# Performance work log

Measured on AMD Instinct MI355X. Metric: run time of the kernel, lower is better.

Reference implementation:

```python
import jax, jax.numpy as jnp
import numpy as np

IN_F, OUT_F, GROUP = 4096, 4096, 128
N_GROUPS = IN_F // GROUP
NIB_SHIFTS = jnp.arange(8, dtype=jnp.int32) * 4  # 8 nibbles per int32


def dequantize(qweight, qzeros, scales, g_idx):
    """GPTQ/exllama 4-bit grouped dequant -> fp16 weight [K, N]."""
    # unpack qweight: [K//8, N] int32 -> [K//8, 8, N] nibbles -> [K, N]
    w_q = (qweight[:, None, :] >> NIB_SHIFTS[None, :, None]) & 0xF
    w_q = w_q.reshape(-1, qweight.shape[1])  # [K, N]
    # unpack qzeros: [G, N//8] int32 -> [G, N//8, 8] -> [G, N]
    z_q = (qzeros[:, :, None] >> NIB_SHIFTS[None, None, :]) & 0xF
    z_q = z_q.reshape(qzeros.shape[0], -1)  # [G, N]
    # exllama stores zero-points minus one: w = (q - (z + 1)) * scale
    z_rows = z_q[g_idx]            # [K, N] int32
    s_rows = scales[g_idx]         # [K, N] fp16
    return (w_q - z_rows - 1).astype(jnp.float16) * s_rows


def setup_inputs() -> dict:
    key = jax.random.key(0)
    k_x, k_qw, k_qz, k_s, k_b = jax.random.split(key, 5)
    x = jax.random.normal(k_x, (4, 2048, IN_F), dtype=jnp.float16)
    qweight = jax.random.randint(k_qw, (IN_F // 8, OUT_F), 0, 2147483647, dtype=jnp.int32)
    qzeros = jax.random.randint(k_qz, (N_GROUPS, OUT_F // 8), 0, 2147483647, dtype=jnp.int32)
    scales = (jax.random.uniform(k_s, (N_GROUPS, OUT_F), dtype=jnp.float32) * 0.01 + 0.001).astype(jnp.float16)
    g_idx = (jnp.arange(IN_F, dtype=jnp.int32) // GROUP).astype(jnp.int32)
    bias = (jax.random.normal(k_b, (OUT_F,), dtype=jnp.float32) * 0.02).astype(jnp.float16)
    return {"x": x, "qweight": qweight, "qzeros": qzeros, "scales": scales, "g_idx": g_idx, "bias": bias}


def reference(x, qweight, qzeros, scales, g_idx, bias):
    W = dequantize(qweight, qzeros, scales, g_idx)      # [K, N] fp16
    lead = x.shape[:-1]
    out = jnp.dot(x.reshape(-1, x.shape[-1]), W)        # fp16 GEMM, [T, N]
    out = out + bias
    return out.reshape(lead + (W.shape[1],))
```

## Files before the change

### kernel.cpp

```cpp
#include <hip/hip_runtime.h>
#include <hip/hip_bf16.h>
#include <stdint.h>

#define M_TOT 8192
#define N_TOT 4096
#define K_TOT 4096
#define GROUP 128


using f32x4  = __attribute__((ext_vector_type(4))) float;
using bf16x8 = __attribute__((ext_vector_type(8))) __bf16;

typedef __attribute__((address_space(3))) void as3_void;
typedef const __attribute__((address_space(1))) void as1_void;

__global__ __launch_bounds__(256) void prep(
    const float* __restrict__ x,
    const int*   __restrict__ qweight,
    const int*   __restrict__ qzeros,
    const float* __restrict__ scales,
    const int*   __restrict__ g_idx,
    __bf16* __restrict__ xb,
    __bf16* __restrict__ Wt)
{
    const int tid = threadIdx.x;
    if (blockIdx.x < 4096) {
        __shared__ __align__(16) unsigned short T[64 * 72];
        const int k0 = (blockIdx.x & 63) * 64;
        const int n0 = (blockIdx.x >> 6) * 64;
        const int g  = g_idx[k0];

        #pragma unroll
        for (int i = 0; i < 2; ++i) {
            const int idx = tid + i * 256;
            const int r   = idx >> 6;
            const int n   = idx & 63;
            const int qi  = qweight[(size_t)((k0 >> 3) + r) * N_TOT + n0 + n];
            const int zi  = qzeros[g * (N_TOT / 8) + ((n0 + n) >> 3)];
            const float s = scales[g * N_TOT + n0 + n];
            const float zs = (float)(((zi >> ((n & 7) * 4)) & 0xF) + 1) * s;
            bf16x8 v;
            #pragma unroll
            for (int j = 0; j < 8; ++j)
                v[j] = (__bf16)((float)((qi >> (4 * j)) & 0xF) * s - zs);
            *(bf16x8*)&T[n * 72 + r * 8] = v;
        }
        __syncthreads();

        const int n = tid >> 2;
        const int c = (tid & 3) * 16;
        const bf16x8 a = *(const bf16x8*)&T[n * 72 + c];
        const bf16x8 b = *(const bf16x8*)&T[n * 72 + c + 8];
        __bf16* dst = Wt + (size_t)(n0 + n) * K_TOT + k0 + c;
        *(bf16x8*)dst = a;
        *(bf16x8*)(dst + 8) = b;
    } else {
        const size_t t = (size_t)(blockIdx.x - 4096) * 256 + tid;
        const f32x4 f0 = __builtin_nontemporal_load((const f32x4*)(x + t * 8));
        const f32x4 f1 = __builtin_nontemporal_load((const f32x4*)(x + t * 8) + 1);
        bf16x8 v;
        v[0]=(__bf16)f0.x; v[1]=(__bf16)f0.y; v[2]=(__bf16)f0.z; v[3]=(__bf16)f0.w;
        v[4]=(__bf16)f1.x; v[5]=(__bf16)f1.y; v[6]=(__bf16)f1.z; v[7]=(__bf16)f1.w;
        *(bf16x8*)(xb + t * 8) = v;
    }
}

#define GBM 256
#define GBN 256
#define GBK 64
#define NKT (K_TOT / GBK)

#define BAR() do { asm volatile("" ::: "memory"); \
                   __builtin_amdgcn_s_barrier();  \
                   asm volatile("" ::: "memory"); } while (0)
#define WAIT_VM4()   asm volatile("s_waitcnt vmcnt(4)"   ::: "memory")
#define WAIT_VM0()   asm volatile("s_waitcnt vmcnt(0)"   ::: "memory")

#define GPHASE(q, STAGE_STMT, TAIL_STMT)                                      \
    {                                                                         \
        bf16x8 av[2][2];                                                      \
        _Pragma("unroll")                                                     \
        for (int ks = 0; ks < 2; ++ks) {                                      \
            av[0][ks] = ldfrag(&Abuf[buf][0], wm, 2 * (q), ks);               \
            av[1][ks] = ldfrag(&Abuf[buf][0], wm, 2 * (q) + 1, ks);           \
        }                                                                     \
        STAGE_STMT;                                                           \
        BAR();                                                                \
        __builtin_amdgcn_s_setprio(1);                                        \
        _Pragma("unroll")                                                     \
        for (int ks = 0; ks < 2; ++ks)                                        \
            _Pragma("unroll")                                                 \
            for (int mtl = 0; mtl < 2; ++mtl)                                 \
                _Pragma("unroll")                                             \
                for (int nt = 0; nt < 4; ++nt)                                \
                    acc[2 * (q) + mtl][nt] =                                  \
                        __builtin_amdgcn_mfma_f32_16x16x32_bf16(              \
                            av[mtl][ks], bv[nt][ks], acc[2 * (q) + mtl][nt],  \
                            0, 0, 0);                                         \
        __builtin_amdgcn_s_setprio(0);                                        \
        TAIL_STMT;                                                            \
        BAR();                                                                \
    }

__global__ __launch_bounds__(512, 2) void gemm8p(
    const __bf16* __restrict__ xb,
    const __bf16* __restrict__ Wt,
    const float*  __restrict__ bias,
    float* __restrict__ out)
{
    __shared__ __align__(16) unsigned short Abuf[2][GBM * GBK];
    __shared__ __align__(16) unsigned short Bbuf[2][GBM * GBK];

    const int tid  = threadIdx.x;
    const int wid  = tid >> 6;
    const int lane = tid & 63;
    const int l15  = lane & 15;
    const int quad = lane >> 4;

    int bid = blockIdx.x;
    bid = (bid & 7) * (512 >> 3) + (bid >> 3);
    const int tn = bid & (N_TOT / GBN - 1);
    const int tm = bid >> 4;
    const int m0 = tm * GBM;
    const int n0 = tn * GBN;

    const int wm = (wid >> 2) * 128;
    const int wn = (wid & 3) * 64;

    f32x4 acc[8][4];
    #pragma unroll
    for (int i = 0; i < 8; ++i)
        #pragma unroll
        for (int j = 0; j < 4; ++j)
            acc[i][j] = (f32x4)0.f;

    auto stage = [&](unsigned short* ldsb, int h,
                     const __bf16* __restrict__ base, int row0, int kt) {
        #pragma unroll
        for (int j = 0; j < 2; ++j) {
            const int c  = j * 512 + tid;
            const int rl = c >> 3;
            const int kc = (c & 7) ^ (rl & 7);
            const __bf16* ga = base + (size_t)(row0 + h * 128 + rl) * K_TOT
                             + kt * GBK + kc * 8;
            __builtin_amdgcn_global_load_lds((as1_void*)ga,
                (as3_void*)&ldsb[h * 8192 + (j * 512 + wid * 64) * 8],
                16, 0, 0);
        }
    };
    auto ldfrag = [&](const unsigned short* ldsb, int wbase, int mt,
                      int ks) -> bf16x8 {
        const int r = wbase + mt * 16 + l15;
        return *(const bf16x8*)
            &ldsb[r * GBK + (((ks * 4 + quad) ^ (r & 7)) << 3)];
    };

    stage(&Abuf[0][0], 0, xb, m0, 0); stage(&Abuf[0][0], 1, xb, m0, 0);
    stage(&Bbuf[0][0], 0, Wt, n0, 0); stage(&Bbuf[0][0], 1, Wt, n0, 0);
    stage(&Bbuf[1][0], 0, Wt, n0, 1); stage(&Bbuf[1][0], 1, Wt, n0, 1);
    WAIT_VM4();
    BAR();

    bf16x8 bv[4][2];

    for (int t = 0; t < NKT; ++t) {
        const int buf = t & 1;

        {
            #pragma unroll
            for (int nt = 0; nt < 4; ++nt)
                #pragma unroll
                for (int ks = 0; ks < 2; ++ks)
                    bv[nt][ks] = ldfrag(&Bbuf[buf][0], wn, nt, ks);
            bf16x8 av[2][2];
            #pragma unroll
            for (int ks = 0; ks < 2; ++ks) {
                av[0][ks] = ldfrag(&Abuf[buf][0], wm, 0, ks);
                av[1][ks] = ldfrag(&Abuf[buf][0], wm, 1, ks);
            }
            if (t + 1 < NKT) stage(&Abuf[buf ^ 1][0], 0, xb, m0, t + 1);
            BAR();
            __builtin_amdgcn_s_setprio(1);
            #pragma unroll
            for (int ks = 0; ks < 2; ++ks)
                #pragma unroll
                for (int mtl = 0; mtl < 2; ++mtl)
                    #pragma unroll
                    for (int nt = 0; nt < 4; ++nt)
                        acc[mtl][nt] = __builtin_amdgcn_mfma_f32_16x16x32_bf16(
                            av[mtl][ks], bv[nt][ks], acc[mtl][nt], 0, 0, 0);
            __builtin_amdgcn_s_setprio(0);
            BAR();
        }
        GPHASE(1, if (t + 1 < NKT) stage(&Abuf[buf ^ 1][0], 1, xb, m0, t + 1), );
        GPHASE(2, if (t + 2 < NKT) stage(&Bbuf[buf][0], 0, Wt, n0, t + 2), );
        GPHASE(3, if (t + 2 < NKT) stage(&Bbuf[buf][0], 1, Wt, n0, t + 2),
               if (t < NKT - 2) { WAIT_VM4(); } else { WAIT_VM0(); });
    }

    #pragma unroll
    for (int nt = 0; nt < 4; ++nt) {
        const int col = n0 + wn + nt * 16 + l15;
        const float bb = bias[col];
        #pragma unroll
        for (int mt = 0; mt < 8; ++mt) {
            const int rowb = m0 + wm + mt * 16 + quad * 4;
            #pragma unroll
            for (int i = 0; i < 4; ++i)
                out[(size_t)(rowb + i) * N_TOT + col] = acc[mt][nt][i] + bb;
        }
    }
}

#define FBM 256
#define FBN 128
#define FBKP 72

__global__ __launch_bounds__(256, 2) void gptq_gemm_fused(
    const float* __restrict__ x, const int* __restrict__ qweight,
    const int* __restrict__ qzeros, const float* __restrict__ scales,
    const int* __restrict__ g_idx, const float* __restrict__ bias,
    float* __restrict__ out)
{
    __shared__ __align__(16) unsigned short As[FBM * FBKP];
    __shared__ __align__(16) unsigned short Bt[FBN * FBKP];

    const int tid  = threadIdx.x;
    const int wave = tid >> 6;
    const int lane = tid & 63;
    const int n0 = blockIdx.x * FBN;
    const int m0 = blockIdx.y * FBM;
    const int wm = (wave >> 1) * 64;
    const int wn = (wave & 1) * 64;
    const int l15  = lane & 15;
    const int quad = lane >> 4;

    f32x4 acc[2][4][4];
    #pragma unroll
    for (int mi = 0; mi < 2; ++mi)
        #pragma unroll
        for (int i = 0; i < 4; ++i)
            #pragma unroll
            for (int j = 0; j < 4; ++j)
                acc[mi][i][j] = (f32x4)0.f;

    const int nb  = tid & 31;
    const int r   = tid >> 5;
    const int zsh = (nb & 7) * 4;

    for (int kt = 0; kt < K_TOT / 64; ++kt) {
        const int k0 = kt * 64;
        #pragma unroll
        for (int i = 0; i < 8; ++i) {
            const int c   = tid + i * 256;
            const int row = c >> 3;
            const int cb  = (c & 7) << 3;
            const float* xp = x + (size_t)(m0 + row) * K_TOT + (k0 + cb);
            const float4 f0 = *(const float4*)xp;
            const float4 f1 = *(const float4*)(xp + 4);
            bf16x8 v;
            v[0]=(__bf16)f0.x; v[1]=(__bf16)f0.y; v[2]=(__bf16)f0.z; v[3]=(__bf16)f0.w;
            v[4]=(__bf16)f1.x; v[5]=(__bf16)f1.y; v[6]=(__bf16)f1.z; v[7]=(__bf16)f1.w;
            *(bf16x8*)&As[row * FBKP + cb] = v;
        }
        const int g    = g_idx[k0];
        const int qrow = (k0 >> 3) + r;
        #pragma unroll
        for (int dn = 0; dn < 4; ++dn) {
            const int n  = nb + dn * 32;
            const int qi = qweight[(size_t)qrow * N_TOT + (n0 + n)];
            const int zi = qzeros[g * (N_TOT / 8) + ((n0 + n) >> 3)];
            const float s = scales[g * N_TOT + (n0 + n)];
            const float zs = (float)(((zi >> zsh) & 0xF) + 1) * s;
            bf16x8 v;
            #pragma unroll
            for (int j = 0; j < 8; ++j)
                v[j] = (__bf16)((float)((qi >> (4 * j)) & 0xF) * s - zs);
            *(bf16x8*)&Bt[n * FBKP + r * 8] = v;
        }
        __syncthreads();
        #pragma unroll
        for (int ks = 0; ks < 2; ++ks) {
            bf16x8 bvv[4];
            #pragma unroll
            for (int nt = 0; nt < 4; ++nt)
                bvv[nt] = *(const bf16x8*)&Bt[(wn + nt * 16 + l15) * FBKP + ks * 32 + quad * 8];
            #pragma unroll
            for (int mi = 0; mi < 2; ++mi) {
                bf16x8 av[4];
                #pragma unroll
                for (int mt = 0; mt < 4; ++mt)
                    av[mt] = *(const bf16x8*)&As[(mi * 128 + wm + mt * 16 + l15) * FBKP + ks * 32 + quad * 8];
                #pragma unroll
                for (int mt = 0; mt < 4; ++mt)
                    #pragma unroll
                    for (int nt = 0; nt < 4; ++nt)
                        acc[mi][mt][nt] = __builtin_amdgcn_mfma_f32_16x16x32_bf16(
                            av[mt], bvv[nt], acc[mi][mt][nt], 0, 0, 0);
            }
        }
        __syncthreads();
    }
    #pragma unroll
    for (int mi = 0; mi < 2; ++mi)
        #pragma unroll
        for (int nt = 0; nt < 4; ++nt) {
            const int col = n0 + wn + nt * 16 + l15;
            const float bvv = bias[col];
            #pragma unroll
            for (int mt = 0; mt < 4; ++mt) {
                const int rowb = m0 + mi * 128 + wm + mt * 16 + quad * 4;
                #pragma unroll
                for (int i = 0; i < 4; ++i)
                    out[(size_t)(rowb + i) * N_TOT + col] = acc[mi][mt][nt][i] + bvv;
            }
        }
}

extern "C" void kernel_launch(void* const* d_in, const int* in_sizes, int n_in,
                              void* d_out, int out_size, void* d_ws, size_t ws_size,
                              hipStream_t stream) {
    const float* x  = (const float*)d_in[0];
    const int*   qw = (const int*)d_in[1];
    const int*   qz = (const int*)d_in[2];
    const float* sc = (const float*)d_in[3];
    const int*   gi = (const int*)d_in[4];
    const float* bs = (const float*)d_in[5];
    float* out = (float*)d_out;

    const size_t xb_bytes = (size_t)M_TOT * K_TOT * 2;
    const size_t wt_bytes = (size_t)N_TOT * K_TOT * 2;

    if (ws_size >= xb_bytes + wt_bytes) {
        __bf16* xb = (__bf16*)d_ws;
        __bf16* Wt = (__bf16*)((char*)d_ws + xb_bytes);
        const int cast_blocks = (M_TOT * K_TOT) / (256 * 8);
        prep<<<dim3(4096 + cast_blocks), dim3(256), 0, stream>>>(
            x, qw, qz, sc, gi, xb, Wt);
        gemm8p<<<dim3((M_TOT / GBM) * (N_TOT / GBN)), dim3(512), 0, stream>>>(
            xb, Wt, bs, out);
    } else {
        gptq_gemm_fused<<<dim3(N_TOT / FBN, M_TOT / FBM), dim3(256), 0, stream>>>(
            x, qw, qz, sc, gi, bs, out);
    }
}
```

Measured before the change: 472.5 us.

## Restructure GEMM main loop with full double-buffering and register-prefetched A fragments

Both A and B tiles are now fully double-buffered, with stage t+2 loaded into the current buffer after it is consumed. Previously A used a one-step lookahead split across phases. A-fragment reads are ping-ponged between two register sets, so each phase's LDS reads overlap the previous phase's MFMAs, and an explicit lgkmcnt wait is added. This deepens the prefetch distance to hide global-load latency, at the cost of more registers and a vmcnt threshold that now depends on the exact count of in-flight loads.

```diff
diff --git a/kernel.cpp b/kernel.cpp
--- a/kernel.cpp
+++ b/kernel.cpp
@@ -73,34 +73,9 @@
 #define BAR() do { asm volatile("" ::: "memory"); \
                    __builtin_amdgcn_s_barrier();  \
                    asm volatile("" ::: "memory"); } while (0)
-#define WAIT_VM4()   asm volatile("s_waitcnt vmcnt(4)"   ::: "memory")
+#define WAIT_LGKM0() asm volatile("s_waitcnt lgkmcnt(0)" ::: "memory")
+#define WAIT_VM8()   asm volatile("s_waitcnt vmcnt(8)"   ::: "memory")
 #define WAIT_VM0()   asm volatile("s_waitcnt vmcnt(0)"   ::: "memory")
-
-#define GPHASE(q, STAGE_STMT, TAIL_STMT)                                      \
-    {                                                                         \
-        bf16x8 av[2][2];                                                      \
-        _Pragma("unroll")                                                     \
-        for (int ks = 0; ks < 2; ++ks) {                                      \
-            av[0][ks] = ldfrag(&Abuf[buf][0], wm, 2 * (q), ks);               \
-            av[1][ks] = ldfrag(&Abuf[buf][0], wm, 2 * (q) + 1, ks);           \
-        }                                                                     \
-        STAGE_STMT;                                                           \
-        BAR();                                                                \
-        __builtin_amdgcn_s_setprio(1);                                        \
-        _Pragma("unroll")                                                     \
-        for (int ks = 0; ks < 2; ++ks)                                        \
-            _Pragma("unroll")                                                 \
-            for (int mtl = 0; mtl < 2; ++mtl)                                 \
-                _Pragma("unroll")                                             \
-                for (int nt = 0; nt < 4; ++nt)                                \
-                    acc[2 * (q) + mtl][nt] =                                  \
-                        __builtin_amdgcn_mfma_f32_16x16x32_bf16(              \
-                            av[mtl][ks], bv[nt][ks], acc[2 * (q) + mtl][nt],  \
-                            0, 0, 0);                                         \
-        __builtin_amdgcn_s_setprio(0);                                        \
-        TAIL_STMT;                                                            \
-        BAR();                                                                \
-    }
 
 __global__ __launch_bounds__(512, 2) void gemm8p(
     const __bf16* __restrict__ xb,
@@ -108,8 +83,7 @@
     const float*  __restrict__ bias,
     float* __restrict__ out)
 {
-    __shared__ __align__(16) unsigned short Abuf[2][GBM * GBK];
-    __shared__ __align__(16) unsigned short Bbuf[2][GBM * GBK];
+    __shared__ __align__(16) unsigned short LDS[2][2][GBM * GBK];
 
     const int tid  = threadIdx.x;
     const int wid  = tid >> 6;
@@ -134,7 +108,7 @@
         for (int j = 0; j < 4; ++j)
             acc[i][j] = (f32x4)0.f;
 
-    auto stage = [&](unsigned short* ldsb, int h,
+    auto stage = [&](int bf, int mat, int h,
                      const __bf16* __restrict__ base, int row0, int kt) {
         #pragma unroll
         for (int j = 0; j < 2; ++j) {
@@ -144,24 +118,25 @@
             const __bf16* ga = base + (size_t)(row0 + h * 128 + rl) * K_TOT
                              + kt * GBK + kc * 8;
             __builtin_amdgcn_global_load_lds((as1_void*)ga,
-                (as3_void*)&ldsb[h * 8192 + (j * 512 + wid * 64) * 8],
+                (as3_void*)&LDS[bf][mat][h * 8192 + (j * 512 + wid * 64) * 8],
                 16, 0, 0);
         }
     };
-    auto ldfrag = [&](const unsigned short* ldsb, int wbase, int mt,
-                      int ks) -> bf16x8 {
+    auto ldfrag = [&](int bf, int mat, int wbase, int mt, int ks) -> bf16x8 {
         const int r = wbase + mt * 16 + l15;
         return *(const bf16x8*)
-            &ldsb[r * GBK + (((ks * 4 + quad) ^ (r & 7)) << 3)];
+            &LDS[bf][mat][r * GBK + (((ks * 4 + quad) ^ (r & 7)) << 3)];
     };
 
-    stage(&Abuf[0][0], 0, xb, m0, 0); stage(&Abuf[0][0], 1, xb, m0, 0);
-    stage(&Bbuf[0][0], 0, Wt, n0, 0); stage(&Bbuf[0][0], 1, Wt, n0, 0);
-    stage(&Bbuf[1][0], 0, Wt, n0, 1); stage(&Bbuf[1][0], 1, Wt, n0, 1);
-    WAIT_VM4();
+    stage(0, 0, 0, xb, m0, 0); stage(0, 0, 1, xb, m0, 0);
+    stage(0, 1, 0, Wt, n0, 0); stage(0, 1, 1, Wt, n0, 0);
+    stage(1, 0, 0, xb, m0, 1); stage(1, 0, 1, xb, m0, 1);
+    stage(1, 1, 0, Wt, n0, 1); stage(1, 1, 1, Wt, n0, 1);
+    WAIT_VM8();
     BAR();
 
     bf16x8 bv[4][2];
+    bf16x8 avA[2][2], avB[2][2];
 
     for (int t = 0; t < NKT; ++t) {
         const int buf = t & 1;
@@ -171,15 +146,16 @@
             for (int nt = 0; nt < 4; ++nt)
                 #pragma unroll
                 for (int ks = 0; ks < 2; ++ks)
-                    bv[nt][ks] = ldfrag(&Bbuf[buf][0], wn, nt, ks);
-            bf16x8 av[2][2];
+                    bv[nt][ks] = ldfrag(buf, 1, wn, nt, ks);
             #pragma unroll
             for (int ks = 0; ks < 2; ++ks) {
-                av[0][ks] = ldfrag(&Abuf[buf][0], wm, 0, ks);
-                av[1][ks] = ldfrag(&Abuf[buf][0], wm, 1, ks);
-            }
-            if (t + 1 < NKT) stage(&Abuf[buf ^ 1][0], 0, xb, m0, t + 1);
-            BAR();
+                avA[0][ks] = ldfrag(buf, 0, wm, 0, ks);
+                avA[1][ks] = ldfrag(buf, 0, wm, 1, ks);
+                avB[0][ks] = ldfrag(buf, 0, wm, 2, ks);
+                avB[1][ks] = ldfrag(buf, 0, wm, 3, ks);
+            }
+            BAR();
+            WAIT_LGKM0();
             __builtin_amdgcn_s_setprio(1);
             #pragma unroll
             for (int ks = 0; ks < 2; ++ks)
@@ -188,14 +164,72 @@
                     #pragma unroll
                     for (int nt = 0; nt < 4; ++nt)
                         acc[mtl][nt] = __builtin_amdgcn_mfma_f32_16x16x32_bf16(
-                            av[mtl][ks], bv[nt][ks], acc[mtl][nt], 0, 0, 0);
+                            avA[mtl][ks], bv[nt][ks], acc[mtl][nt], 0, 0, 0);
             __builtin_amdgcn_s_setprio(0);
             BAR();
         }
-        GPHASE(1, if (t + 1 < NKT) stage(&Abuf[buf ^ 1][0], 1, xb, m0, t + 1), );
-        GPHASE(2, if (t + 2 < NKT) stage(&Bbuf[buf][0], 0, Wt, n0, t + 2), );
-        GPHASE(3, if (t + 2 < NKT) stage(&Bbuf[buf][0], 1, Wt, n0, t + 2),
-               if (t < NKT - 2) { WAIT_VM4(); } else { WAIT_VM0(); });
+        {
+            #pragma unroll
+            for (int ks = 0; ks < 2; ++ks) {
+                avA[0][ks] = ldfrag(buf, 0, wm, 4, ks);
+                avA[1][ks] = ldfrag(buf, 0, wm, 5, ks);
+            }
+            if (t + 2 < NKT) stage(buf, 1, 0, Wt, n0, t + 2);
+            BAR();
+            WAIT_LGKM0();
+            __builtin_amdgcn_s_setprio(1);
+            #pragma unroll
+            for (int ks = 0; ks < 2; ++ks)
+                #pragma unroll
+                for (int mtl = 0; mtl < 2; ++mtl)
+                    #pragma unroll
+                    for (int nt = 0; nt < 4; ++nt)
+                        acc[2 + mtl][nt] = __builtin_amdgcn_mfma_f32_16x16x32_bf16(
+                            avB[mtl][ks], bv[nt][ks], acc[2 + mtl][nt], 0, 0, 0);
+            __builtin_amdgcn_s_setprio(0);
+            BAR();
+        }
+        {
+            #pragma unroll
+            for (int ks = 0; ks < 2; ++ks) {
+                avB[0][ks] = ldfrag(buf, 0, wm, 6, ks);
+                avB[1][ks] = ldfrag(buf, 0, wm, 7, ks);
+            }
+            if (t + 2 < NKT) stage(buf, 1, 1, Wt, n0, t + 2);
+            BAR();
+            WAIT_LGKM0();
+            __builtin_amdgcn_s_setprio(1);
+            #pragma unroll
+            for (int ks = 0; ks < 2; ++ks)
+                #pragma unroll
+                for (int mtl = 0; mtl < 2; ++mtl)
+                    #pragma unroll
+                    for (int nt = 0; nt < 4; ++nt)
+                        acc[4 + mtl][nt] = __builtin_amdgcn_mfma_f32_16x16x32_bf16(
+                            avA[mtl][ks], bv[nt][ks], acc[4 + mtl][nt], 0, 0, 0);
+            __builtin_amdgcn_s_setprio(0);
+            BAR();
+        }
+        {
+            if (t + 2 < NKT) {
+                stage(buf, 0, 0, xb, m0, t + 2);
+                stage(buf, 0, 1, xb, m0, t + 2);
+            }
+            BAR();
+            WAIT_LGKM0();
+            __builtin_amdgcn_s_setprio(1);
+            #pragma unroll
+            for (int ks = 0; ks < 2; ++ks)
+                #pragma unroll
+                for (int mtl = 0; mtl < 2; ++mtl)
+                    #pragma unroll
+                    for (int nt = 0; nt < 4; ++nt)
+                        acc[6 + mtl][nt] = __builtin_amdgcn_mfma_f32_16x16x32_bf16(
+                            avB[mtl][ks], bv[nt][ks], acc[6 + mtl][nt], 0, 0, 0);
+            __builtin_amdgcn_s_setprio(0);
+            BAR();
+        }
+        if (t < NKT - 2) { WAIT_VM8(); } else { WAIT_VM0(); }
     }
 
     #pragma unroll
```

Result: faster. 458.0 us (-3.1%).
